# Kernel optimization log

Hardware: AMD Instinct MI355X
Metric: run time of the kernel (lower is better)

Reference implementation:

```python
import jax, jax.numpy as jnp
import numpy as np

HIDDEN = 64
N_NODES = 100000
N_EDGES = 1250000
EDGE_FEAT = 13


def setup_inputs() -> dict:
    key = jax.random.key(0)
    ks = jax.random.split(key, 16)
    d = HIDDEN
    inp = {
        'x': jax.random.normal(ks[0], (N_NODES, d), dtype=jnp.float32),
        'edge_index': jax.random.randint(ks[1], (2, N_EDGES), 0, N_NODES, dtype=jnp.int64),
        'edge_attr': jax.random.uniform(ks[2], (N_EDGES, EDGE_FEAT), dtype=jnp.float32),
        # learned params
        'aaaaa': jax.random.normal(ks[3], (EDGE_FEAT, 1), dtype=jnp.float32) * 0.5,
        'W1': jax.random.normal(ks[4], (d, d), dtype=jnp.float32) / np.sqrt(d),
        'b1': jnp.zeros((d,), dtype=jnp.float32),
        'W2': jax.random.normal(ks[5], (d, d), dtype=jnp.float32) / np.sqrt(d),
        'b2': jnp.zeros((d,), dtype=jnp.float32),
        'W3': jax.random.normal(ks[6], (d, d), dtype=jnp.float32) / np.sqrt(d),
        'b3': jnp.zeros((d,), dtype=jnp.float32),
        'wg1': jax.random.normal(ks[7], (d, 1), dtype=jnp.float32) / np.sqrt(d),
        'bg1': jnp.zeros((1,), dtype=jnp.float32),
        'wg2': jax.random.normal(ks[8], (d, 1), dtype=jnp.float32) / np.sqrt(d),
        'bg2': jnp.zeros((1,), dtype=jnp.float32),
        'wg3': jax.random.normal(ks[9], (d, 1), dtype=jnp.float32) / np.sqrt(d),
        'bg3': jnp.zeros((1,), dtype=jnp.float32),
    }
    return inp


def _gcn_norm(edge_index, edge_weight, num_nodes):
    # PyG gcn_norm: add self-loops (weight 1), symmetric deg^{-1/2} normalization
    loop = jnp.arange(num_nodes, dtype=edge_index.dtype)
    rows = jnp.concatenate([edge_index[0], loop])
    cols = jnp.concatenate([edge_index[1], loop])
    w = jnp.concatenate([edge_weight, jnp.ones((num_nodes,), edge_weight.dtype)])
    deg = jax.ops.segment_sum(w, cols, num_segments=num_nodes)
    dinv = jnp.where(deg > 0, jax.lax.rsqrt(jnp.where(deg > 0, deg, 1.0)), 0.0)
    norm = dinv[rows] * w * dinv[cols]
    return rows, cols, norm


def _gcn_layer(x, W, b, rows, cols, norm, num_nodes):
    h = x @ W  # transform first (out_dim == in_dim)
    msg = norm[:, None] * h[rows]          # gather + scale  [E+N, d]
    out = jnp.zeros_like(h).at[cols].add(msg)  # scatter-add aggregation
    return out + b


def _att_pool(x, wg, bg):
    # GlobalAttention with single graph (batch all zeros):
    # gate = sigmoid(Linear(x)); softmax over nodes; weighted sum
    gate = jax.nn.sigmoid(x @ wg + bg)      # [N, 1]
    a = jax.nn.softmax(gate, axis=0)        # softmax over node dim
    return jnp.sum(a * x, axis=0, keepdims=True)  # [1, d]


def reference(x, edge_index, edge_attr, aaaaa, W1, b1, W2, b2, W3, b3,
              wg1, bg1, wg2, bg2, wg3, bg3):
    num_nodes = x.shape[0]
    edge_weight = (edge_attr @ jax.nn.softmax(aaaaa, axis=0)).reshape(-1)  # [E]
    rows, cols, norm = _gcn_norm(edge_index, edge_weight, num_nodes)

    x1 = jax.nn.relu(_gcn_layer(x, W1, b1, rows, cols, norm, num_nodes))
    r1 = _att_pool(x1, wg1, bg1)
    x2 = jax.nn.relu(_gcn_layer(x1, W2, b2, rows, cols, norm, num_nodes))
    r2 = _att_pool(x2, wg2, bg2)
    x3 = jax.nn.relu(_gcn_layer(x2, W3, b3, rows, cols, norm, num_nodes))
    r3 = _att_pool(x3, wg3, bg3)
    return jnp.concatenate([r1, r2, r3], axis=1)  # [1, 3*hidden]
```

## Files before the change

kernel.cpp:

```cpp
#include <hip/hip_runtime.h>
#include <hip/hip_bf16.h>
#include <math.h>

#define HIDDEN    64
#define N_NODES   100000
#define N_EDGES   1250000
#define EDGE_FEAT 13

#define GATHER_BLOCKS 2048
#define GEMM_ROWS 64
#define GEMM_NB   ((N_NODES + GEMM_ROWS - 1) / GEMM_ROWS)

#define NBKT    391
#define BCAP    4096
#define A_EPB   512
#define NBLKA   ((N_EDGES + A_EPB - 1) / A_EPB)
#define CPT     ((NBLKA + 255) / 256)

typedef unsigned short bf16_t;
typedef unsigned char  u8;
typedef unsigned short u16;
typedef unsigned int   u32;
typedef unsigned long long u64;
typedef float f32x2 __attribute__((ext_vector_type(2)));

#if defined(__has_builtin)
# if __has_builtin(__builtin_amdgcn_cvt_f32_fp8)
#  define USE_HW_FP8 1
# endif
# if __has_builtin(__builtin_amdgcn_cvt_pk_f32_fp8)
#  define USE_HW_FP8PK 1
# endif
#endif

static __device__ __forceinline__ float bf2f(bf16_t u) {
    union { unsigned int i; float f; } x; x.i = ((unsigned int)u) << 16; return x.f;
}
static __device__ __forceinline__ bf16_t f2bf(float f) {
    union { float f; unsigned int i; } u; u.f = f;
    unsigned int r = u.i + 0x7FFFu + ((u.i >> 16) & 1u);
    return (bf16_t)(r >> 16);
}

static __device__ __forceinline__ u8 f2fp8(float f) {
    union { float f; unsigned int u; } v; v.f = f;
    unsigned int s = (v.u >> 31) << 7;
    unsigned int mag = v.u & 0x7fffffffu;
    if (mag >= 0x43E80000u) return (u8)(s | 0x7Eu);
    if (mag < 0x3C800000u) {
        union { unsigned int u; float f; } t; t.u = mag;
        int qi = (int)rintf(t.f * 512.0f);
        return (u8)(s | (unsigned int)qi);
    }
    unsigned int r = mag + 0x7FFFFu + ((mag >> 20) & 1u);
    unsigned int e8 = (r >> 23) - 120u;
    unsigned int m3 = (r >> 20) & 7u;
    return (u8)(s | (e8 << 3) | m3);
}

static __device__ __forceinline__ float fp8dec(u32 b) {
#ifdef USE_HW_FP8
    return __builtin_amdgcn_cvt_f32_fp8(b, 0);
#else
    u32 m = b & 0x7Fu;
    u32 sgn = (b & 0x80u) << 24;
    union { u32 u; float f; } fn; fn.u = 0x3C000000u + (m << 20);
    float mg = (m < 8u) ? (float)m * (1.0f / 512.0f) : fn.f;
    union { float f; u32 u; } r; r.f = mg; r.u |= sgn;
    return r.f;
#endif
}

static __device__ __forceinline__ void fp8x4dec(u32 w, float* f) {
#ifdef USE_HW_FP8PK
    f32x2 lo = __builtin_amdgcn_cvt_pk_f32_fp8(w, false);
    f32x2 hi = __builtin_amdgcn_cvt_pk_f32_fp8(w, true);
    f[0] = lo.x; f[1] = lo.y; f[2] = hi.x; f[3] = hi.y;
#else
    f[0] = fp8dec(w & 0xFFu);
    f[1] = fp8dec((w >> 8) & 0xFFu);
    f[2] = fp8dec((w >> 16) & 0xFFu);
    f[3] = fp8dec((w >> 24) & 0xFFu);
#endif
}

#define OFF_TOT    0
#define OFF_GBASE  2048
#define OFF_BLKH   4096
#define OFF_BLKE   3824640
#define OFF_VST    7645184
#define OFF_START  7645184
#define OFF_DINV   8045184
#define OFF_ACC    8445184
#define OFF_POOLP  8446208
#define OFF_REC    10043648
#define OFF_H8     17645184
#define OFF_A      24045184
#define OFF_BREC   OFF_H8

__global__ __launch_bounds__(256) void wqk_kernel(
    const float* __restrict__ attr, const int* __restrict__ rows,
    const int* __restrict__ cols, const float* __restrict__ aaaaa,
    u64* __restrict__ vstash, int* __restrict__ blkHist, int E)
{
    __shared__ float s[16];
    __shared__ int hist[NBKT];
    __shared__ float astage[4][EDGE_FEAT * 64];
    int t = threadIdx.x, blk = blockIdx.x;
    int lane = t & 63, wid = t >> 6;
    if (t == 0) {
        float m = -1e30f;
        for (int i = 0; i < EDGE_FEAT; i++) m = fmaxf(m, aaaaa[i]);
        float ex[EDGE_FEAT]; float sum = 0.f;
        for (int i = 0; i < EDGE_FEAT; i++) { ex[i] = __expf(aaaaa[i] - m); sum += ex[i]; }
        float inv = 1.f / sum;
        for (int i = 0; i < EDGE_FEAT; i++) s[i] = ex[i] * inv;
    }
    for (int b = t; b < NBKT; b += 256) hist[b] = 0;
    __syncthreads();

    float sw[EDGE_FEAT];
#pragma unroll
    for (int f = 0; f < EDGE_FEAT; f++) sw[f] = s[f];

    float* as = astage[wid];
    int wbase = blk * A_EPB + wid * (A_EPB / 4);
#pragma unroll 1
    for (int c = 0; c < A_EPB / 4 / 64; c++) {
        int ebase = wbase + c * 64;
        int rem = E - ebase;
        if (rem <= 0) break;
        int limw = min(64, rem) * EDGE_FEAT;
        size_t gb = (size_t)ebase * EDGE_FEAT;
#pragma unroll
        for (int j = 0; j < EDGE_FEAT; j++) {
            int idx = lane + j * 64;
            if (idx < limw) as[idx] = attr[gb + idx];
        }
        int e = ebase + lane;
        if (e < E) {
            const float* rowp = &as[lane * EDGE_FEAT];
            float acc = 0.f;
#pragma unroll
            for (int f = 0; f < EDGE_FEAT; f++) acc = fmaf(rowp[f], sw[f], acc);
            u32 wq = min((u32)(fmaxf(acc, 0.f) * 32768.0f), 32767u);
            u32 cc = (u32)cols[e], rr = (u32)rows[e];
            int rk = atomicAdd(&hist[cc >> 8], 1);
            vstash[e] = ((u64)(u32)rk << 49) | ((u64)wq << 34) | ((u64)cc << 17) | (u64)rr;
        }
    }
    __syncthreads();
    for (int b = t; b < NBKT; b += 256) blkHist[blk * NBKT + b] = hist[b];
}

__global__ __launch_bounds__(256) void colscan_kernel(
    const int* __restrict__ blkHist, int* __restrict__ blkExcl,
    int* __restrict__ bucketTot)
{
    __shared__ int sc[256];
    int t = threadIdx.x, b = blockIdx.x;
    int loc[CPT]; int lsum = 0;
#pragma unroll
    for (int i = 0; i < CPT; i++) {
        int k = t * CPT + i;
        int v = (k < NBLKA) ? blkHist[(size_t)k * NBKT + b] : 0;
        loc[i] = lsum; lsum += v;
    }
    sc[t] = lsum;
    __syncthreads();
    for (int off = 1; off < 256; off <<= 1) {
        int a = (t >= off) ? sc[t - off] : 0;
        __syncthreads();
        sc[t] += a;
        __syncthreads();
    }
    int excl = sc[t] - lsum;
#pragma unroll
    for (int i = 0; i < CPT; i++) {
        int k = t * CPT + i;
        if (k < NBLKA) blkExcl[(size_t)k * NBKT + b] = excl + loc[i];
    }
    if (t == 255) bucketTot[b] = sc[255];
}

__global__ void bscan(const int* __restrict__ bucketTot, int* __restrict__ gbase) {
    __shared__ int sc[512];
    int t = threadIdx.x;
    int v0 = (t < NBKT) ? bucketTot[t] : 0;
    int v1 = (t + 256 < NBKT) ? bucketTot[t + 256] : 0;
    sc[t] = v0; sc[t + 256] = v1;
    __syncthreads();
    for (int off = 1; off < 512; off <<= 1) {
        int a0 = (t >= off) ? sc[t - off] : 0;
        int a1 = sc[t + 256 - off];
        __syncthreads();
        sc[t] += a0; sc[t + 256] += a1;
        __syncthreads();
    }
    if (t < NBKT) gbase[t] = sc[t] - v0;
    if (t + 256 < NBKT) gbase[t + 256] = sc[t + 256] - v1;
}

__global__ __launch_bounds__(256) void scat_kernel(
    const u64* __restrict__ vstash, const int* __restrict__ blkHist,
    const int* __restrict__ blkExcl, u64* __restrict__ brec, int E)
{
    __shared__ u64 lbuf[A_EPB];
    __shared__ int hist[NBKT];
    __shared__ int exg[NBKT];
    __shared__ int cex[512];
    int t = threadIdx.x, blk = blockIdx.x;
    for (int b = t; b < NBKT; b += 256) {
        hist[b] = blkHist[(size_t)blk * NBKT + b];
        exg[b]  = blkExcl[(size_t)blk * NBKT + b];
    }
    __syncthreads();
    cex[t]       = (t < NBKT) ? hist[t] : 0;
    cex[t + 256] = (t + 256 < NBKT) ? hist[t + 256] : 0;
    __syncthreads();
    for (int off = 1; off < 512; off <<= 1) {
        int a0 = (t >= off) ? cex[t - off] : 0;
        int a1 = cex[t + 256 - off];
        __syncthreads();
        cex[t] += a0; cex[t + 256] += a1;
        __syncthreads();
    }

    int e0 = blk * A_EPB;
    int blkcnt = min(A_EPB, E - e0);
    for (int c = 0; c < A_EPB / 256; c++) {
        int e = e0 + c * 256 + t;
        if (e < E) {
            u64 v = vstash[e];
            int b = (int)((v >> 25) & 0x1FFu);
            int rk = (int)(v >> 49);
            lbuf[cex[b] - hist[b] + rk] = v;
        }
    }
    __syncthreads();
    for (int i = t; i < blkcnt; i += 256) {
        u64 w = lbuf[i];
        int b = (int)((w >> 25) & 0x1FFu);
        int ex = cex[b] - hist[b];
        int slot = exg[b] + (i - ex);
        if (slot < BCAP)
            brec[(size_t)b * BCAP + slot] = w;
    }
}

__global__ __launch_bounds__(256) void sortb_kernel(
    const u64* __restrict__ brec,
    const int* __restrict__ bucketTot, const int* __restrict__ gbase,
    u32* __restrict__ recp, int* __restrict__ startA,
    float* __restrict__ dinv, int N)
{
    __shared__ int hist[256];
    __shared__ int isum[256];
    __shared__ int incl[256];
    __shared__ u16 rnk[BCAP];
    __shared__ u64 buf[BCAP];
    int t = threadIdx.x;
    int b = blockIdx.x;
    int cnt = min(bucketTot[b], BCAP);
    int gb = gbase[b];
    int cbase = b << 8;
    int ncols = min(256, N - cbase);
    hist[t] = 0; isum[t] = 0;
    __syncthreads();

    for (int i = t; i < cnt; i += 256) {
        u64 v = brec[(size_t)b * BCAP + i];
        buf[i] = v;
        int c = (int)((v >> 17) & 255u);
        int wq = (int)((v >> 34) & 0x7FFFu);
        rnk[i] = (u16)atomicAdd(&hist[c], 1);
        atomicAdd(&isum[c], wq);
    }
    __syncthreads();

    incl[t] = hist[t];
    __syncthreads();
    for (int off = 1; off < 256; off <<= 1) {
        int a0 = (t >= off) ? incl[t - off] : 0;
        __syncthreads();
        incl[t] += a0;
        __syncthreads();
    }
    if (t < ncols) {
        startA[cbase + t] = gb + (incl[t] - hist[t]);
        dinv[cbase + t] = rsqrtf(1.0f + (float)isum[t] * (1.0f / 32768.0f));
    }
    __syncthreads();

    for (int i = t; i < cnt; i += 256) {
        u64 v = buf[i];
        int c = (int)((v >> 17) & 255u);
        int ex = incl[c] - hist[c];
        u32 row = (u32)(v & 0x1FFFFu);
        u32 wq = (u32)((v >> 34) & 0x7FFFu);
        recp[gb + ex + rnk[i]] = (row << 15) | wq;
    }
}

template <typename T> struct Feat;
template <> struct Feat<float> {
    static __device__ __forceinline__ float4 ld4(const float* A, size_t off) {
        return *(const float4*)(A + off);
    }
};
template <> struct Feat<bf16_t> {
    static __device__ __forceinline__ float4 ld4(const bf16_t* A, size_t off) {
        uint2 v = *(const uint2*)(A + off);
        float4 r;
        r.x = bf2f((bf16_t)(v.x & 0xffffu));
        r.y = bf2f((bf16_t)(v.x >> 16));
        r.z = bf2f((bf16_t)(v.y & 0xffffu));
        r.w = bf2f((bf16_t)(v.y >> 16));
        return r;
    }
};

template <typename TIn>
__global__ __launch_bounds__(256) void gemm64(const TIn* __restrict__ A,
                                              const float* __restrict__ W,
                                              const float* __restrict__ dinv,
                                              u8* __restrict__ H8, int N) {
    __shared__ float Ws[HIDDEN * HIDDEN];
    int tid = threadIdx.x;
    {
        const float4* Wv = (const float4*)W;
        float4* Sv = (float4*)Ws;
#pragma unroll
        for (int i = 0; i < 4; i++) Sv[tid + 256 * i] = Wv[tid + 256 * i];
    }
    __syncthreads();
    int rg = tid >> 4;
    int c0 = (tid & 15) * 4;
    int rbase = blockIdx.x * GEMM_ROWS + rg;
    int rld[4]; bool rok[4];
#pragma unroll
    for (int i = 0; i < 4; i++) {
        int r = rbase + 16 * i;
        rok[i] = (r < N);
        rld[i] = rok[i] ? r : 0;
    }
    float acc[4][4];
#pragma unroll
    for (int i = 0; i < 4; i++)
#pragma unroll
        for (int j = 0; j < 4; j++) acc[i][j] = 0.f;

    for (int k = 0; k < HIDDEN; k += 4) {
        float4 a4[4];
#pragma unroll
        for (int i = 0; i < 4; i++)
            a4[i] = Feat<TIn>::ld4(A, (size_t)rld[i] * HIDDEN + k);
#pragma unroll
        for (int kk = 0; kk < 4; kk++) {
            float4 w4 = *(const float4*)(&Ws[(k + kk) * HIDDEN + c0]);
            float wv[4] = {w4.x, w4.y, w4.z, w4.w};
#pragma unroll
            for (int i = 0; i < 4; i++) {
                float ak[4] = {a4[i].x, a4[i].y, a4[i].z, a4[i].w};
                float av = ak[kk];
#pragma unroll
                for (int j = 0; j < 4; j++) acc[i][j] = fmaf(av, wv[j], acc[i][j]);
            }
        }
    }
#pragma unroll
    for (int i = 0; i < 4; i++) {
        if (!rok[i]) continue;
        float dv = dinv[rld[i]];
        unsigned int b0 = f2fp8(dv * acc[i][0]);
        unsigned int b1 = f2fp8(dv * acc[i][1]);
        unsigned int b2 = f2fp8(dv * acc[i][2]);
        unsigned int b3 = f2fp8(dv * acc[i][3]);
        *(u32*)(H8 + (size_t)rld[i] * HIDDEN + c0) =
            b0 | (b1 << 8) | (b2 << 16) | (b3 << 24);
    }
}

__global__ __launch_bounds__(256) void gather_pool_kernel(
    const u8* __restrict__ h8,
    const int* __restrict__ start,
    const u32* __restrict__ recp,
    const float* __restrict__ dinv, const float* __restrict__ bias,
    const float* __restrict__ wg, const float* __restrict__ bg,
    bf16_t* __restrict__ out, float* __restrict__ poolpart, int N)
{
    __shared__ float sred[4][65];
    int lane  = threadIdx.x & 63;
    int wid   = threadIdx.x >> 6;
    int eslot = lane >> 4;
    int ch4   = (lane & 15) * 4;
    int wave = blockIdx.x * 4 + wid;
    const int nwaves = GATHER_BLOCKS * 4;
    float4 wgv = *(const float4*)(wg + ch4);
    float4 bv4 = *(const float4*)(bias + ch4);
    float bg0 = bg[0];
    float accv[4] = {0.f, 0.f, 0.f, 0.f};
    float accs = 0.f;

    for (int n = wave; n < N; n += nwaves) {
        int s = start[n];
        int e2 = (n + 1 < N) ? start[n + 1] : N_EDGES;
        float di = dinv[n];
        float a[4] = {0.f, 0.f, 0.f, 0.f};
        for (int base = s; base < e2; base += 64) {
            int cnt64 = min(e2 - base, 64);
            u32 rv = recp[base + min(lane, cnt64 - 1)];
            for (int j = 0; j < cnt64; j += 8) {
                int q0 = j + eslot, q1 = j + 4 + eslot;
                u32 p0 = (u32)__shfl((int)rv, q0 & 63, 64);
                u32 p1 = (u32)__shfl((int)rv, q1 & 63, 64);
                float w0 = (q0 < cnt64) ? (float)(p0 & 0x7FFFu) : 0.f;
                float w1 = (q1 < cnt64) ? (float)(p1 & 0x7FFFu) : 0.f;
                u32 off0 = ((p0 & 0xFFFF8000u) >> 9) + (u32)ch4;
                u32 off1 = ((p1 & 0xFFFF8000u) >> 9) + (u32)ch4;
                u32 d0 = *(const u32*)(h8 + off0);
                u32 d1 = *(const u32*)(h8 + off1);
                float h0[4], h1[4];
                fp8x4dec(d0, h0);
                fp8x4dec(d1, h1);
#pragma unroll
                for (int i = 0; i < 4; i++) {
                    a[i] = fmaf(w0, h0[i], a[i]);
                    a[i] = fmaf(w1, h1[i], a[i]);
                }
            }
        }
#pragma unroll
        for (int i = 0; i < 4; i++) {
            a[i] += __shfl_xor(a[i], 16, 64);
            a[i] += __shfl_xor(a[i], 32, 64);
        }
        u32 sw = *(const u32*)(h8 + (u32)n * (u32)HIDDEN + (u32)ch4);
        float sf[4];
        fp8x4dec(sw, sf);
        float dis = di * (1.0f / 32768.0f);
        float v[4];
#pragma unroll
        for (int i = 0; i < 4; i++) {
            float t0 = fmaf(dis, a[i], ((const float*)&bv4)[i]);
            v[i] = fmaxf(fmaf(di, sf[i], t0), 0.f);
        }
        if (eslot == 0) {
            u32 lo = (u32)f2bf(v[0]) | ((u32)f2bf(v[1]) << 16);
            u32 hi = (u32)f2bf(v[2]) | ((u32)f2bf(v[3]) << 16);
            *(uint2*)(out + (size_t)n * HIDDEN + ch4) = make_uint2(lo, hi);
        }
        float p = v[0] * wgv.x + v[1] * wgv.y + v[2] * wgv.z + v[3] * wgv.w;
        p += __shfl_xor(p, 1, 64);
        p += __shfl_xor(p, 2, 64);
        p += __shfl_xor(p, 4, 64);
        p += __shfl_xor(p, 8, 64);
        float g = 1.f / (1.f + __expf(-(p + bg0)));
        float eg = __expf(g);
#pragma unroll
        for (int i = 0; i < 4; i++) accv[i] = fmaf(eg, v[i], accv[i]);
        accs += eg;
    }

    if (eslot == 0) {
        sred[wid][ch4 + 0] = accv[0];
        sred[wid][ch4 + 1] = accv[1];
        sred[wid][ch4 + 2] = accv[2];
        sred[wid][ch4 + 3] = accv[3];
    }
    if (lane == 0) sred[wid][64] = accs;
    __syncthreads();
    if (wid == 0) {
        float s0 = sred[0][lane] + sred[1][lane] + sred[2][lane] + sred[3][lane];
        poolpart[(size_t)lane * GATHER_BLOCKS + blockIdx.x] = s0;
        if (lane == 0) {
            float ss = sred[0][64] + sred[1][64] + sred[2][64] + sred[3][64];
            poolpart[(size_t)64 * GATHER_BLOCKS + blockIdx.x] = ss;
        }
    }
}

__global__ void pool_reduce(const float* __restrict__ poolpart, float* __restrict__ acc) {
    int entry = (int)((blockIdx.x * blockDim.x + threadIdx.x) >> 6);
    int lane = threadIdx.x & 63;
    if (entry >= 3 * 65) return;
    const float* p = poolpart + (size_t)entry * GATHER_BLOCKS;
    float s = 0.f;
    for (int i = lane; i < GATHER_BLOCKS; i += 64) s += p[i];
#pragma unroll
    for (int m = 32; m > 0; m >>= 1) s += __shfl_xor(s, m, 64);
    if (lane == 0) acc[entry] = s;
}

__global__ void finalize_kernel(const float* __restrict__ acc, float* __restrict__ out) {
    int i = threadIdx.x;
    if (i >= 3 * HIDDEN) return;
    int layer = i >> 6, c = i & 63;
    const float* a = acc + layer * 65;
    out[i] = a[c] / a[64];
}

extern "C" void kernel_launch(void* const* d_in, const int* in_sizes, int n_in,
                              void* d_out, int out_size, void* d_ws, size_t ws_size,
                              hipStream_t stream) {
    const float* x          = (const float*)d_in[0];
    const int*   edge_index = (const int*)  d_in[1];
    const float* edge_attr  = (const float*)d_in[2];
    const float* aaaaa      = (const float*)d_in[3];
    const float* W1 = (const float*)d_in[4];  const float* b1 = (const float*)d_in[5];
    const float* W2 = (const float*)d_in[6];  const float* b2 = (const float*)d_in[7];
    const float* W3 = (const float*)d_in[8];  const float* b3 = (const float*)d_in[9];
    const float* wg1 = (const float*)d_in[10]; const float* bg1 = (const float*)d_in[11];
    const float* wg2 = (const float*)d_in[12]; const float* bg2 = (const float*)d_in[13];
    const float* wg3 = (const float*)d_in[14]; const float* bg3 = (const float*)d_in[15];
    float* out = (float*)d_out;

    char* ws = (char*)d_ws;
    int*    bucketTot = (int*)   (ws + OFF_TOT);
    int*    gbase     = (int*)   (ws + OFF_GBASE);
    int*    blkHist   = (int*)   (ws + OFF_BLKH);
    int*    blkExcl   = (int*)   (ws + OFF_BLKE);
    u64*    vstash    = (u64*)   (ws + OFF_VST);
    int*    startA    = (int*)   (ws + OFF_START);
    float*  dinv      = (float*) (ws + OFF_DINV);
    float*  acc       = (float*) (ws + OFF_ACC);
    float*  poolpart  = (float*) (ws + OFF_POOLP);
    u32*    recp      = (u32*)   (ws + OFF_REC);
    u8*     h8        = (u8*)    (ws + OFF_H8);
    bf16_t* bufA      = (bf16_t*)(ws + OFF_A);
    u64*    brec      = (u64*)   (ws + OFF_BREC);

    const int* rows = edge_index;
    const int* cols = edge_index + N_EDGES;
    const int N = N_NODES, E = N_EDGES;

    wqk_kernel<<<NBLKA, 256, 0, stream>>>(edge_attr, rows, cols, aaaaa, vstash, blkHist, E);
    colscan_kernel<<<NBKT, 256, 0, stream>>>(blkHist, blkExcl, bucketTot);
    bscan<<<1, 256, 0, stream>>>(bucketTot, gbase);
    scat_kernel<<<NBLKA, 256, 0, stream>>>(vstash, blkHist, blkExcl, brec, E);
    sortb_kernel<<<NBKT, 256, 0, stream>>>(brec, bucketTot, gbase, recp, startA, dinv, N);

    const float* Wm[3]  = {W1, W2, W3};
    const float* bs[3]  = {b1, b2, b3};
    const float* wgs[3] = {wg1, wg2, wg3};
    const float* bgs[3] = {bg1, bg2, bg3};

    for (int l = 0; l < 3; l++) {
        if (l == 0)
            gemm64<float><<<GEMM_NB, 256, 0, stream>>>(x, Wm[l], dinv, h8, N);
        else
            gemm64<bf16_t><<<GEMM_NB, 256, 0, stream>>>(bufA, Wm[l], dinv, h8, N);
        gather_pool_kernel<<<GATHER_BLOCKS, 256, 0, stream>>>(
            h8, startA, recp, dinv, bs[l], wgs[l], bgs[l],
            bufA, poolpart + (size_t)l * 65 * GATHER_BLOCKS, N);
    }

    pool_reduce<<<(3 * 65 * 64 + 255) / 256, 256, 0, stream>>>(poolpart, acc);
    finalize_kernel<<<1, 192, 0, stream>>>(acc, out);
}
```

Baseline: 399.3 us.

## Fuse next-layer GEMM into gather/pool epilogue, double-buffer fp8 features

The gather/pool kernel now multiplies each node's post-ReLU feature vector by the next layer's weight matrix, holding W in registers (16 float4 per lane) and broadcasting via shuffles, then writes dinv-scaled fp8 features directly. This drops the bf16 intermediate buffer and the separate GEMM launches for layers 2 and 3, and two fp8 buffers alternate between layers. In exchange it adds 64 floats of register pressure per lane, plus extra shuffles and FMAs per node inside a latency-bound gather loop, which may lower occupancy.

```diff
diff --git a/kernel.cpp b/kernel.cpp
--- a/kernel.cpp
+++ b/kernel.cpp
@@ -32,15 +32,6 @@
 #  define USE_HW_FP8PK 1
 # endif
 #endif
-
-static __device__ __forceinline__ float bf2f(bf16_t u) {
-    union { unsigned int i; float f; } x; x.i = ((unsigned int)u) << 16; return x.f;
-}
-static __device__ __forceinline__ bf16_t f2bf(float f) {
-    union { float f; unsigned int i; } u; u.f = f;
-    unsigned int r = u.i + 0x7FFFu + ((u.i >> 16) & 1u);
-    return (bf16_t)(r >> 16);
-}
 
 static __device__ __forceinline__ u8 f2fp8(float f) {
     union { float f; unsigned int u; } v; v.f = f;
@@ -94,9 +85,9 @@
 #define OFF_ACC    8445184
 #define OFF_POOLP  8446208
 #define OFF_REC    10043648
-#define OFF_H8     17645184
-#define OFF_A      24045184
-#define OFF_BREC   OFF_H8
+#define OFF_H8A    17645184
+#define OFF_H8B    24045184
+#define OFF_BREC   OFF_H8A
 
 __global__ __launch_bounds__(256) void wqk_kernel(
     const float* __restrict__ attr, const int* __restrict__ rows,
@@ -302,26 +293,7 @@
     }
 }
 
-template <typename T> struct Feat;
-template <> struct Feat<float> {
-    static __device__ __forceinline__ float4 ld4(const float* A, size_t off) {
-        return *(const float4*)(A + off);
-    }
-};
-template <> struct Feat<bf16_t> {
-    static __device__ __forceinline__ float4 ld4(const bf16_t* A, size_t off) {
-        uint2 v = *(const uint2*)(A + off);
-        float4 r;
-        r.x = bf2f((bf16_t)(v.x & 0xffffu));
-        r.y = bf2f((bf16_t)(v.x >> 16));
-        r.z = bf2f((bf16_t)(v.y & 0xffffu));
-        r.w = bf2f((bf16_t)(v.y >> 16));
-        return r;
-    }
-};
-
-template <typename TIn>
-__global__ __launch_bounds__(256) void gemm64(const TIn* __restrict__ A,
+__global__ __launch_bounds__(256) void gemm64(const float* __restrict__ A,
                                               const float* __restrict__ W,
                                               const float* __restrict__ dinv,
                                               u8* __restrict__ H8, int N) {
@@ -354,7 +326,7 @@
         float4 a4[4];
 #pragma unroll
         for (int i = 0; i < 4; i++)
-            a4[i] = Feat<TIn>::ld4(A, (size_t)rld[i] * HIDDEN + k);
+            a4[i] = *(const float4*)(A + (size_t)rld[i] * HIDDEN + k);
 #pragma unroll
         for (int kk = 0; kk < 4; kk++) {
             float4 w4 = *(const float4*)(&Ws[(k + kk) * HIDDEN + c0]);
@@ -381,13 +353,15 @@
     }
 }
 
+template <int FUSE>
 __global__ __launch_bounds__(256) void gather_pool_kernel(
     const u8* __restrict__ h8,
     const int* __restrict__ start,
     const u32* __restrict__ recp,
     const float* __restrict__ dinv, const float* __restrict__ bias,
     const float* __restrict__ wg, const float* __restrict__ bg,
-    bf16_t* __restrict__ out, float* __restrict__ poolpart, int N)
+    const float* __restrict__ Wn, u8* __restrict__ h8n,
+    float* __restrict__ poolpart, int N)
 {
     __shared__ float sred[4][65];
     int lane  = threadIdx.x & 63;
@@ -401,6 +375,13 @@
     float bg0 = bg[0];
     float accv[4] = {0.f, 0.f, 0.f, 0.f};
     float accs = 0.f;
+
+    float4 wn[16];
+    if (FUSE) {
+#pragma unroll
+        for (int j = 0; j < 16; j++)
+            wn[j] = *(const float4*)(Wn + (size_t)(16 * eslot + j) * HIDDEN + ch4);
+    }
 
     for (int n = wave; n < N; n += nwaves) {
         int s = start[n];
@@ -435,9 +416,9 @@
             a[i] += __shfl_xor(a[i], 16, 64);
             a[i] += __shfl_xor(a[i], 32, 64);
         }
-        u32 sw = *(const u32*)(h8 + (u32)n * (u32)HIDDEN + (u32)ch4);
+        u32 swd = *(const u32*)(h8 + (u32)n * (u32)HIDDEN + (u32)ch4);
         float sf[4];
-        fp8x4dec(sw, sf);
+        fp8x4dec(swd, sf);
         float dis = di * (1.0f / 32768.0f);
         float v[4];
 #pragma unroll
@@ -445,11 +426,36 @@
             float t0 = fmaf(dis, a[i], ((const float*)&bv4)[i]);
             v[i] = fmaxf(fmaf(di, sf[i], t0), 0.f);
         }
-        if (eslot == 0) {
-            u32 lo = (u32)f2bf(v[0]) | ((u32)f2bf(v[1]) << 16);
-            u32 hi = (u32)f2bf(v[2]) | ((u32)f2bf(v[3]) << 16);
-            *(uint2*)(out + (size_t)n * HIDDEN + ch4) = make_uint2(lo, hi);
-        }
+
+        if (FUSE) {
+            float y[4] = {0.f, 0.f, 0.f, 0.f};
+#pragma unroll
+            for (int jj = 0; jj < 4; jj++) {
+                int src = 20 * eslot + jj;
+#pragma unroll
+                for (int m = 0; m < 4; m++) {
+                    float vk = __shfl(v[m], src, 64);
+                    const float4 w4 = wn[4 * jj + m];
+                    y[0] = fmaf(vk, w4.x, y[0]);
+                    y[1] = fmaf(vk, w4.y, y[1]);
+                    y[2] = fmaf(vk, w4.z, y[2]);
+                    y[3] = fmaf(vk, w4.w, y[3]);
+                }
+            }
+#pragma unroll
+            for (int m = 0; m < 4; m++) {
+                y[m] += __shfl_xor(y[m], 16, 64);
+                y[m] += __shfl_xor(y[m], 32, 64);
+            }
+            if (eslot == 0) {
+                u32 wd = (u32)f2fp8(di * y[0])
+                       | ((u32)f2fp8(di * y[1]) << 8)
+                       | ((u32)f2fp8(di * y[2]) << 16)
+                       | ((u32)f2fp8(di * y[3]) << 24);
+                *(u32*)(h8n + (size_t)n * HIDDEN + ch4) = wd;
+            }
+        }
+
         float p = v[0] * wgv.x + v[1] * wgv.y + v[2] * wgv.z + v[3] * wgv.w;
         p += __shfl_xor(p, 1, 64);
         p += __shfl_xor(p, 2, 64);
@@ -526,8 +532,8 @@
     float*  acc       = (float*) (ws + OFF_ACC);
     float*  poolpart  = (float*) (ws + OFF_POOLP);
     u32*    recp      = (u32*)   (ws + OFF_REC);
-    u8*     h8        = (u8*)    (ws + OFF_H8);
-    bf16_t* bufA      = (bf16_t*)(ws + OFF_A);
+    u8*     h8a       = (u8*)    (ws + OFF_H8A);
+    u8*     h8b       = (u8*)    (ws + OFF_H8B);
     u64*    brec      = (u64*)   (ws + OFF_BREC);
 
     const int* rows = edge_index;
@@ -540,20 +546,16 @@
     scat_kernel<<<NBLKA, 256, 0, stream>>>(vstash, blkHist, blkExcl, brec, E);
     sortb_kernel<<<NBKT, 256, 0, stream>>>(brec, bucketTot, gbase, recp, startA, dinv, N);
 
-    const float* Wm[3]  = {W1, W2, W3};
-    const float* bs[3]  = {b1, b2, b3};
-    const float* wgs[3] = {wg1, wg2, wg3};
-    const float* bgs[3] = {bg1, bg2, bg3};
-
-    for (int l = 0; l < 3; l++) {
-        if (l == 0)
-            gemm64<float><<<GEMM_NB, 256, 0, stream>>>(x, Wm[l], dinv, h8, N);
-        else
-            gemm64<bf16_t><<<GEMM_NB, 256, 0, stream>>>(bufA, Wm[l], dinv, h8, N);
-        gather_pool_kernel<<<GATHER_BLOCKS, 256, 0, stream>>>(
-            h8, startA, recp, dinv, bs[l], wgs[l], bgs[l],
-            bufA, poolpart + (size_t)l * 65 * GATHER_BLOCKS, N);
-    }
+    gemm64<<<GEMM_NB, 256, 0, stream>>>(x, W1, dinv, h8a, N);
+    gather_pool_kernel<1><<<GATHER_BLOCKS, 256, 0, stream>>>(
+        h8a, startA, recp, dinv, b1, wg1, bg1, W2, h8b,
+        poolpart + (size_t)0 * 65 * GATHER_BLOCKS, N);
+    gather_pool_kernel<1><<<GATHER_BLOCKS, 256, 0, stream>>>(
+        h8b, startA, recp, dinv, b2, wg2, bg2, W3, h8a,
+        poolpart + (size_t)1 * 65 * GATHER_BLOCKS, N);
+    gather_pool_kernel<0><<<GATHER_BLOCKS, 256, 0, stream>>>(
+        h8a, startA, recp, dinv, b3, wg3, bg3, nullptr, nullptr,
+        poolpart + (size_t)2 * 65 * GATHER_BLOCKS, N);
 
     pool_reduce<<<(3 * 65 * 64 + 255) / 256, 256, 0, stream>>>(poolpart, acc);
     finalize_kernel<<<1, 192, 0, stream>>>(acc, out);
```

After: 422.6 us. 5.8% more time.

## Unroll gather loop to four loads in flight; double edges per bucketing block

Applied to the files above, without the earlier changes.

The per-node aggregation loop now processes 16 edges per iteration, issuing four independent fp8 row gathers before decoding and accumulating them, so more memory loads are in flight per wave. Separately, the edge-bucketing kernel handles 1024 edges per block instead of 512, halving the number of blocks and shrinking the per-block histogram scratch; the workspace offsets are recomputed to match. The unroll raises register pressure and wastes more lanes on nodes with few edges, while the larger blocks reduce parallelism in the bucketing phase.

```diff
diff --git a/kernel.cpp b/kernel.cpp
--- a/kernel.cpp
+++ b/kernel.cpp
@@ -13,7 +13,7 @@
 
 #define NBKT    391
 #define BCAP    4096
-#define A_EPB   512
+#define A_EPB   1024
 #define NBLKA   ((N_EDGES + A_EPB - 1) / A_EPB)
 #define CPT     ((NBLKA + 255) / 256)
 
@@ -87,15 +87,15 @@
 #define OFF_TOT    0
 #define OFF_GBASE  2048
 #define OFF_BLKH   4096
-#define OFF_BLKE   3824640
-#define OFF_VST    7645184
-#define OFF_START  7645184
-#define OFF_DINV   8045184
-#define OFF_ACC    8445184
-#define OFF_POOLP  8446208
-#define OFF_REC    10043648
-#define OFF_H8     17645184
-#define OFF_A      24045184
+#define OFF_BLKE   1914880
+#define OFF_VST    3825664
+#define OFF_START  3825664
+#define OFF_DINV   4225664
+#define OFF_ACC    4625664
+#define OFF_POOLP  4626688
+#define OFF_REC    6224128
+#define OFF_H8     13825664
+#define OFF_A      20225664
 #define OFF_BREC   OFF_H8
 
 __global__ __launch_bounds__(256) void wqk_kernel(
@@ -410,23 +410,28 @@
         for (int base = s; base < e2; base += 64) {
             int cnt64 = min(e2 - base, 64);
             u32 rv = recp[base + min(lane, cnt64 - 1)];
-            for (int j = 0; j < cnt64; j += 8) {
-                int q0 = j + eslot, q1 = j + 4 + eslot;
-                u32 p0 = (u32)__shfl((int)rv, q0 & 63, 64);
-                u32 p1 = (u32)__shfl((int)rv, q1 & 63, 64);
-                float w0 = (q0 < cnt64) ? (float)(p0 & 0x7FFFu) : 0.f;
-                float w1 = (q1 < cnt64) ? (float)(p1 & 0x7FFFu) : 0.f;
-                u32 off0 = ((p0 & 0xFFFF8000u) >> 9) + (u32)ch4;
-                u32 off1 = ((p1 & 0xFFFF8000u) >> 9) + (u32)ch4;
-                u32 d0 = *(const u32*)(h8 + off0);
-                u32 d1 = *(const u32*)(h8 + off1);
-                float h0[4], h1[4];
-                fp8x4dec(d0, h0);
-                fp8x4dec(d1, h1);
+            for (int j = 0; j < cnt64; j += 16) {
+                u32 p[4]; float wt[4];
 #pragma unroll
                 for (int i = 0; i < 4; i++) {
-                    a[i] = fmaf(w0, h0[i], a[i]);
-                    a[i] = fmaf(w1, h1[i], a[i]);
+                    int q = j + 4 * i + eslot;
+                    p[i] = (u32)__shfl((int)rv, q & 63, 64);
+                    wt[i] = (q < cnt64) ? (float)(p[i] & 0x7FFFu) : 0.f;
+                }
+                u32 d[4];
+#pragma unroll
+                for (int i = 0; i < 4; i++) {
+                    u32 off = ((p[i] & 0xFFFF8000u) >> 9) + (u32)ch4;
+                    d[i] = *(const u32*)(h8 + off);
+                }
+#pragma unroll
+                for (int i = 0; i < 4; i++) {
+                    float h[4];
+                    fp8x4dec(d[i], h);
+                    a[0] = fmaf(wt[i], h[0], a[0]);
+                    a[1] = fmaf(wt[i], h[1], a[1]);
+                    a[2] = fmaf(wt[i], h[2], a[2]);
+                    a[3] = fmaf(wt[i], h[3], a[3]);
                 }
             }
         }
@@ -435,9 +440,9 @@
             a[i] += __shfl_xor(a[i], 16, 64);
             a[i] += __shfl_xor(a[i], 32, 64);
         }
-        u32 sw = *(const u32*)(h8 + (u32)n * (u32)HIDDEN + (u32)ch4);
+        u32 swd = *(const u32*)(h8 + (u32)n * (u32)HIDDEN + (u32)ch4);
         float sf[4];
-        fp8x4dec(sw, sf);
+        fp8x4dec(swd, sf);
         float dis = di * (1.0f / 32768.0f);
         float v[4];
 #pragma unroll
```

After: 431.3 us. 8.0% more time.
